# Performance work log

Measured on AMD Instinct MI355X. Metric: run time of the kernel, lower is better.

The kernel has to match this reference:

```python
import jax, jax.numpy as jnp
import numpy as np
from jax import lax

# PSTConv constants (match init_kwargs)
R = 0.5            # ball-query radius
K = 32             # neighbors per anchor
SPATIAL_STRIDE = 2
TK = 3             # temporal kernel size (odd)
TSTRIDE = 1        # temporal stride
PAD = (1, 1)       # temporal padding, 'zeros' mode
MID = 128
OUT = 256


def setup_inputs() -> dict:
    key = jax.random.key(0)
    k1, k2, k3, k4, k5 = jax.random.split(key, 5)
    B, L, N, C = 8, 6, 2048, 64
    xyzs = jax.random.uniform(k1, (B, L, N, 3), dtype=jnp.float32)
    features = jax.random.normal(k2, (B, L, C, N), dtype=jnp.float32)
    # kaiming_uniform with size=[mid, in+3, 1, 1]: bound = 1/sqrt(in_planes+3)
    b = 1.0 / np.sqrt(C + 3)
    w_d = jax.random.uniform(k3, (MID, 3), minval=-b, maxval=b, dtype=jnp.float32)
    w_f = jax.random.uniform(k4, (MID, C), minval=-b, maxval=b, dtype=jnp.float32)
    bt = 1.0 / np.sqrt(TK * MID)
    w_t = jax.random.uniform(k5, (OUT, TK * MID), minval=-bt, maxval=bt, dtype=jnp.float32)
    return {"xyzs": xyzs, "features": features, "w_d": w_d, "w_f": w_f, "w_t": w_t}


def _fps(xyz, m):
    # furthest point sampling on [N,3]; CUDA kernel starts from index 0
    N = xyz.shape[0]
    def step(carry, _):
        dists, far = carry
        d = jnp.sum((xyz - xyz[far]) ** 2, axis=-1)
        dists = jnp.minimum(dists, d)
        nxt = jnp.argmax(dists).astype(jnp.int32)
        return (dists, nxt), far
    init = (jnp.full((N,), 1e10, dtype=xyz.dtype), jnp.int32(0))
    _, idx = lax.scan(step, init, None, length=m)
    return idx  # [m] int32


def _ball_query(nbr_xyz, anchor_xyz):
    # nbr_xyz [B,N,3], anchor_xyz [B,M,3] -> [B,M,K] int32 indices into N
    # Semantics of pointnet2 ball_query: first K points (in index order) within
    # radius R; slots past the count are filled with the first found index
    # (0 if no point is in range).
    N = nbr_xyz.shape[1]
    d2 = jnp.sum((anchor_xyz[:, :, None, :] - nbr_xyz[:, None, :, :]) ** 2, axis=-1)  # [B,M,N]
    vals = jnp.where(d2 < R * R, jnp.arange(N, dtype=jnp.int32), jnp.int32(N))
    neg_top, _ = lax.top_k(-vals, K)          # K smallest indices, ascending
    idx = -neg_top                            # [B,M,K]
    first = idx[..., :1]
    fill = jnp.where(first < N, first, 0)
    return jnp.where(idx < N, idx, fill)


def _group(feat, idx):
    # feat [B,C,N], idx [B,M,K] -> [B,C,M,K]
    return jax.vmap(lambda f, i: f[:, i])(feat, idx)


def reference(xyzs, features, w_d, w_f, w_t):
    B, L, N, _ = xyzs.shape
    M = N // SPATIAL_STRIDE
    rad = TK // 2
    # zero temporal padding
    zx = jnp.zeros((B, 1, N, 3), xyzs.dtype)
    zf = jnp.zeros((B, 1, features.shape[2], N), features.dtype)
    xp = jnp.concatenate([zx] * PAD[0] + [xyzs] + [zx] * PAD[1], axis=1)
    fp = jnp.concatenate([zf] * PAD[0] + [features] + [zf] * PAD[1], axis=1)
    Lp = L + PAD[0] + PAD[1]

    new_xyzs, new_feats = [], []
    fps_b = jax.vmap(lambda x: _fps(x, M))
    for t in range(rad, Lp - rad, TSTRIDE):
        xyz_t = xp[:, t]                                   # [B,N,3]
        aidx = fps_b(xyz_t)                                # [B,M]
        anchor = jnp.take_along_axis(xyz_t, aidx[:, :, None], axis=1)  # [B,M,3]
        anchor_c = jnp.transpose(anchor, (0, 2, 1))[:, :, :, None]     # [B,3,M,1]
        sfs = []
        for i in range(t - rad, t + rad + 1):
            idx = _ball_query(xp[:, i], anchor)            # [B,M,K]
            g_xyz = _group(jnp.transpose(xp[:, i], (0, 2, 1)), idx)    # [B,3,M,K]
            disp = g_xyz - anchor_c
            d = jnp.einsum('oc,bcmk->bomk', w_d, disp)     # [B,MID,M,K]
            g_f = _group(fp[:, i], idx)                    # [B,C,M,K]
            f = jnp.einsum('oc,bcmk->bomk', w_f, g_f)
            sfs.append(jnp.max(f + d, axis=-1))            # [B,MID,M]
        sf = jax.nn.relu(jnp.concatenate(sfs, axis=1))     # [B,TK*MID,M]
        new_feats.append(jnp.einsum('oc,bcm->bom', w_t, sf))
        new_xyzs.append(anchor)
    return jnp.stack(new_xyzs, axis=1), jnp.stack(new_feats, axis=1)
```

## Files before the change

kernel.cpp:

```cpp
#include <hip/hip_runtime.h>

#define BATCH 8
#define LFRM  6
#define NP    2048
#define MP    1024
#define CIN   64
#define MIDC  128
#define OUTC  256
#define TKM   384
#define KNN   32
#define RAD2  0.25f

#define FPS_BLOCKS (BATCH * LFRM)
#define FT_BLOCKS  (BATCH * LFRM * (NP / 64))
#define WFS 132

typedef float f2 __attribute__((ext_vector_type(2)));
typedef float f32x4 __attribute__((ext_vector_type(4)));
typedef _Float16 f16x8 __attribute__((ext_vector_type(8)));
typedef _Float16 f16x4 __attribute__((ext_vector_type(4)));

union SharedU {
  struct {
    float4 pts[NP];
    unsigned long long wk[2][4];
  } fps;
  struct {
    float ftile[CIN][64];
    float wfT[CIN][WFS];
    float xt[64], yt[64], zt[64];
    float wdl[MIDC * 3];
  } ft;
};

__device__ __forceinline__ uint64_t kmax64(uint64_t a, uint64_t b) {
  return a > b ? a : b;
}
template <int CTRL>
__device__ __forceinline__ uint64_t key_dpp(uint64_t k) {
  int lo = __builtin_amdgcn_update_dpp((int)(uint32_t)k, (int)(uint32_t)k,
                                       CTRL, 0xF, 0xF, false);
  int hi = __builtin_amdgcn_update_dpp((int)(uint32_t)(k >> 32),
                                       (int)(uint32_t)(k >> 32),
                                       CTRL, 0xF, 0xF, false);
  return ((uint64_t)(uint32_t)hi << 32) | (uint32_t)lo;
}
__device__ __forceinline__ uint64_t key_swz16(uint64_t k) {
  int lo = __builtin_amdgcn_ds_swizzle((int)(uint32_t)k, 0x401F);
  int hi = __builtin_amdgcn_ds_swizzle((int)(uint32_t)(k >> 32), 0x401F);
  return ((uint64_t)(uint32_t)hi << 32) | (uint32_t)lo;
}
__device__ __forceinline__ uint64_t key_x32(uint64_t k) {
  int lo = __shfl_xor((int)(uint32_t)k, 32);
  int hi = __shfl_xor((int)(uint32_t)(k >> 32), 32);
  return ((uint64_t)(uint32_t)hi << 32) | (uint32_t)lo;
}

__device__ __forceinline__ void fps_path(const float* __restrict__ xyzs,
                                         float* __restrict__ out_xyz,
                                         SharedU* sh) {
#pragma clang fp contract(off)
  const int bt = blockIdx.x;
  const int tid = threadIdx.x;
  const int lane = tid & 63, wv = tid >> 6;
  const float* src = xyzs + (size_t)bt * NP * 3;

  for (int q = tid; q < NP; q += 256)
    sh->fps.pts[q] = make_float4(src[q * 3 + 0], src[q * 3 + 1], src[q * 3 + 2], 0.f);
  __syncthreads();

  f2 px[4], py[4], pz[4], dist[4];
#pragma unroll
  for (int u = 0; u < 4; ++u) {
    float4 a = sh->fps.pts[(wv * 8 + 2 * u) * 64 + lane];
    float4 b = sh->fps.pts[(wv * 8 + 2 * u + 1) * 64 + lane];
    px[u] = f2{a.x, b.x};
    py[u] = f2{a.y, b.y};
    pz[u] = f2{a.z, b.z};
    dist[u] = f2{1e10f, 1e10f};
  }

  float4 p0 = sh->fps.pts[0];
  float fx = p0.x, fy = p0.y, fz = p0.z;
  float* dst = out_xyz + (size_t)bt * MP * 3;

  for (int it = 0; it < MP; ++it) {
    if (tid == 0) {
      dst[it * 3 + 0] = fx;
      dst[it * 3 + 1] = fy;
      dst[it * 3 + 2] = fz;
    }
    const f2 fx2 = {fx, fx}, fy2 = {fy, fy}, fz2 = {fz, fz};
    float bv = -1.0f;
    int bsu = 0;
#pragma unroll
    for (int u = 0; u < 4; ++u) {
      f2 dx = px[u] - fx2;
      f2 dy = py[u] - fy2;
      f2 dz = pz[u] - fz2;
      f2 m = dx * dx;
      m = m + dy * dy;
      m = m + dz * dz;
      f2 nd = __builtin_elementwise_min(dist[u], m);
      dist[u] = nd;
      bool cx = nd.x > bv;
      bv = cx ? nd.x : bv;
      bsu = cx ? 2 * u : bsu;
      bool cy = nd.y > bv;
      bv = cy ? nd.y : bv;
      bsu = cy ? 2 * u + 1 : bsu;
    }
    const uint32_t p = (uint32_t)(((wv * 8 + bsu) << 6) | lane);
    uint64_t key = ((uint64_t)__float_as_uint(bv) << 32) | (uint32_t)(~p);
    key = kmax64(key, key_dpp<0x121>(key));
    key = kmax64(key, key_dpp<0x122>(key));
    key = kmax64(key, key_dpp<0x124>(key));
    key = kmax64(key, key_dpp<0x128>(key));
    key = kmax64(key, key_swz16(key));
    key = kmax64(key, key_x32(key));

    const int par = it & 1;
    if (lane == 0) sh->fps.wk[par][wv] = key;
    __syncthreads();
    uint64_t k0 = kmax64(sh->fps.wk[par][0], sh->fps.wk[par][1]);
    uint64_t k1 = kmax64(sh->fps.wk[par][2], sh->fps.wk[par][3]);
    uint64_t kg = kmax64(k0, k1);
    const uint32_t wp = ~(uint32_t)kg;
    float4 w = sh->fps.pts[wp];
    fx = w.x; fy = w.y; fz = w.z;
  }
}

__device__ __forceinline__ void ftrans_path(const float* __restrict__ features,
                                            const float* __restrict__ w_f,
                                            const float* __restrict__ w_d,
                                            const float* __restrict__ xyzs,
                                            float* __restrict__ G,
                                            SharedU* sh) {
  const int blk = blockIdx.x - FPS_BLOCKS;
  const int ntile = blk & 31;
  const int bl = blk >> 5;
  const int tid = threadIdx.x;

  const float* fsrc = features + (size_t)bl * CIN * NP + (size_t)ntile * 64;
  for (int idx = tid; idx < CIN * 64; idx += 256) {
    int c = idx >> 6, n = idx & 63;
    sh->ft.ftile[c][n] = fsrc[(size_t)c * NP + n];
  }
  for (int idx = tid; idx < CIN * MIDC; idx += 256) {
    int c = idx & 63, o = idx >> 6;
    sh->ft.wfT[c][o] = w_f[o * CIN + c];
  }
  if (tid < 64) {
    const float* xs = xyzs + ((size_t)bl * NP + (size_t)ntile * 64 + tid) * 3;
    sh->ft.xt[tid] = xs[0];
    sh->ft.yt[tid] = xs[1];
    sh->ft.zt[tid] = xs[2];
  }
  for (int idx = tid; idx < MIDC * 3; idx += 256) sh->ft.wdl[idx] = w_d[idx];
  __syncthreads();

  const int op = tid & 31;
  const int ng = tid >> 5;
  const int ob = op * 4;
  const int nb = ng * 8;

  float acc[4][8];
#pragma unroll
  for (int oo = 0; oo < 4; ++oo) {
    const float w0 = sh->ft.wdl[(ob + oo) * 3 + 0];
    const float w1 = sh->ft.wdl[(ob + oo) * 3 + 1];
    const float w2 = sh->ft.wdl[(ob + oo) * 3 + 2];
#pragma unroll
    for (int j = 0; j < 8; ++j)
      acc[oo][j] = w0 * sh->ft.xt[nb + j] + w1 * sh->ft.yt[nb + j] +
                   w2 * sh->ft.zt[nb + j];
  }

#pragma unroll 4
  for (int c = 0; c < CIN; ++c) {
    const float4 wq = *(const float4*)&sh->ft.wfT[c][ob];
    const float4 fA = *(const float4*)&sh->ft.ftile[c][nb];
    const float4 fB = *(const float4*)&sh->ft.ftile[c][nb + 4];
    const float wo[4] = {wq.x, wq.y, wq.z, wq.w};
    const float fv[8] = {fA.x, fA.y, fA.z, fA.w, fB.x, fB.y, fB.z, fB.w};
#pragma unroll
    for (int oo = 0; oo < 4; ++oo)
#pragma unroll
      for (int j = 0; j < 8; ++j)
        acc[oo][j] += wo[oo] * fv[j];
  }

  float* dstp = G + ((size_t)bl * NP + (size_t)ntile * 64) * MIDC;
#pragma unroll
  for (int j = 0; j < 8; ++j) {
    float4 v = make_float4(acc[0][j], acc[1][j], acc[2][j], acc[3][j]);
    *(float4*)&dstp[(size_t)(nb + j) * MIDC + ob] = v;
  }
}

__global__ __launch_bounds__(256, 1) void fps_ftrans_kernel(
    const float* __restrict__ xyzs, const float* __restrict__ features,
    const float* __restrict__ w_f, const float* __restrict__ w_d,
    float* __restrict__ out_xyz, float* __restrict__ G) {
  __shared__ SharedU sh;
  if (blockIdx.x < FPS_BLOCKS) {
    fps_path(xyzs, out_xyz, &sh);
    return;
  }
  ftrans_path(features, w_f, w_d, xyzs, G, &sh);
}

#define PSTR 392

__global__ __launch_bounds__(256) void pst_main(const float* __restrict__ xyzs,
                                                const float* __restrict__ w_d,
                                                const float* __restrict__ w_t,
                                                const float* __restrict__ G,
                                                const float* __restrict__ anchors,
                                                float* __restrict__ out_feat) {
  __shared__ union {
    float pxyz[NP * 3];
    _Float16 sf[32][PSTR];
  } u;
  __shared__ unsigned short nidx[32][KNN];
  __shared__ float anc[32][3];

  const int blk = blockIdx.x;
  const int mt = blk & 31;
  const int bt = blk >> 5;
  const int b = bt / LFRM;
  const int t = bt % LFRM + 1;
  const int tid = threadIdx.x;

  const float* asrc = anchors + ((size_t)bt * MP + (size_t)mt * 32) * 3;
  if (tid < 96) anc[tid / 3][tid % 3] = asrc[tid];
  __syncthreads();

  const int al = tid >> 3;
  const int j = tid & 7;
  const float ax = anc[al][0], ay = anc[al][1], az = anc[al][2];

  float wda[16];
#pragma unroll
  for (int c4 = 0; c4 < 4; ++c4)
#pragma unroll
    for (int r = 0; r < 4; ++r) {
      int o = c4 * 32 + j * 4 + r;
      wda[c4 * 4 + r] = w_d[o * 3 + 0] * ax + w_d[o * 3 + 1] * ay +
                        w_d[o * 3 + 2] * az;
    }

  const int lane = tid & 63, wv = tid >> 6;

  f16x4 hreg[3][4];

#pragma unroll
  for (int ii = 0; ii < 3; ++ii) {
    const int i = t - 1 + ii;

    if (i == 0 || i == LFRM + 1) {
#pragma unroll
      for (int c4 = 0; c4 < 4; ++c4) {
        f16x4 h;
#pragma unroll
        for (int r = 0; r < 4; ++r)
          h[r] = (_Float16)fmaxf(-wda[c4 * 4 + r], 0.f);
        hreg[ii][c4] = h;
      }
    } else {
      const int f2i = i - 1;
      const float* fxyz = xyzs + (size_t)(b * LFRM + f2i) * NP * 3;
      __syncthreads();
      for (int q = tid; q < NP * 3; q += 256) u.pxyz[q] = fxyz[q];
      __syncthreads();

      for (int aa = 0; aa < 8; ++aa) {
        const int a = wv * 8 + aa;
        const float qx = anc[a][0], qy = anc[a][1], qz = anc[a][2];
        int total = 0;
        int fillidx = 0;
        for (int ch = 0; ch < NP / 64; ++ch) {
          const int p = ch * 64 + lane;
          float d2;
          {
#pragma clang fp contract(off)
            float dx = qx - u.pxyz[p * 3 + 0];
            float dy = qy - u.pxyz[p * 3 + 1];
            float dz = qz - u.pxyz[p * 3 + 2];
            d2 = dx * dx + dy * dy + dz * dz;
          }
          const bool inb = d2 < RAD2;
          const unsigned long long mk = __ballot(inb);
          if (mk != 0ull && total == 0)
            fillidx = ch * 64 + (int)__builtin_ctzll(mk);
          const int before = (int)__builtin_popcountll(mk & ((1ull << lane) - 1ull));
          const int slot = total + before;
          if (inb && slot < KNN) nidx[a][slot] = (unsigned short)p;
          total += (int)__builtin_popcountll(mk);
          if (total >= KNN) break;
        }
        const int nf = total < KNN ? total : KNN;
        if (lane < KNN - nf) nidx[a][nf + lane] = (unsigned short)fillidx;
      }

      const float* gf = G + (size_t)(b * LFRM + f2i) * NP * MIDC;
      float mg[16];
#pragma unroll
      for (int uq = 0; uq < 16; ++uq) mg[uq] = -1e30f;
#pragma unroll 4
      for (int k = 0; k < KNN; ++k) {
        const int p = nidx[al][k];
        const float* rowp = gf + (size_t)p * MIDC + j * 4;
#pragma unroll
        for (int c4 = 0; c4 < 4; ++c4) {
          float4 v = *(const float4*)(rowp + c4 * 32);
          mg[c4 * 4 + 0] = fmaxf(mg[c4 * 4 + 0], v.x);
          mg[c4 * 4 + 1] = fmaxf(mg[c4 * 4 + 1], v.y);
          mg[c4 * 4 + 2] = fmaxf(mg[c4 * 4 + 2], v.z);
          mg[c4 * 4 + 3] = fmaxf(mg[c4 * 4 + 3], v.w);
        }
      }
#pragma unroll
      for (int c4 = 0; c4 < 4; ++c4) {
        f16x4 h;
#pragma unroll
        for (int r = 0; r < 4; ++r)
          h[r] = (_Float16)fmaxf(mg[c4 * 4 + r] - wda[c4 * 4 + r], 0.f);
        hreg[ii][c4] = h;
      }
    }
  }

  __syncthreads();
#pragma unroll
  for (int ii = 0; ii < 3; ++ii)
#pragma unroll
    for (int c4 = 0; c4 < 4; ++c4)
      *(f16x4*)&u.sf[al][ii * MIDC + c4 * 32 + j * 4] = hreg[ii][c4];
  __syncthreads();

  const int l16 = lane & 15, lq = lane >> 4;
  f32x4 accm[4][2];
#pragma unroll
  for (int q = 0; q < 4; ++q)
#pragma unroll
    for (int n2 = 0; n2 < 2; ++n2) accm[q][n2] = f32x4{0.f, 0.f, 0.f, 0.f};

  for (int kc = 0; kc < TKM / 32; ++kc) {
    f16x8 bfr[2];
#pragma unroll
    for (int n2 = 0; n2 < 2; ++n2)
      bfr[n2] = *(const f16x8*)&u.sf[n2 * 16 + l16][kc * 32 + lq * 8];
#pragma unroll
    for (int q = 0; q < 4; ++q) {
      const int row = (wv * 4 + q) * 16 + l16;
      const float4* ap = (const float4*)(w_t + (size_t)row * TKM + kc * 32 + lq * 8);
      float4 a0 = ap[0], a1 = ap[1];
      f16x8 afr;
      afr[0] = (_Float16)a0.x; afr[1] = (_Float16)a0.y;
      afr[2] = (_Float16)a0.z; afr[3] = (_Float16)a0.w;
      afr[4] = (_Float16)a1.x; afr[5] = (_Float16)a1.y;
      afr[6] = (_Float16)a1.z; afr[7] = (_Float16)a1.w;
      accm[q][0] = __builtin_amdgcn_mfma_f32_16x16x32_f16(afr, bfr[0], accm[q][0], 0, 0, 0);
      accm[q][1] = __builtin_amdgcn_mfma_f32_16x16x32_f16(afr, bfr[1], accm[q][1], 0, 0, 0);
    }
  }

  float* ob = out_feat + (size_t)bt * OUTC * MP + (size_t)mt * 32;
#pragma unroll
  for (int q = 0; q < 4; ++q) {
    const int orow = (wv * 4 + q) * 16 + lq * 4;
#pragma unroll
    for (int n2 = 0; n2 < 2; ++n2)
#pragma unroll
      for (int r = 0; r < 4; ++r)
        ob[(size_t)(orow + r) * MP + n2 * 16 + l16] = accm[q][n2][r];
  }
}

extern "C" void kernel_launch(void* const* d_in, const int* in_sizes, int n_in,
                              void* d_out, int out_size, void* d_ws, size_t ws_size,
                              hipStream_t stream) {
  const float* xyzs = (const float*)d_in[0];
  const float* features = (const float*)d_in[1];
  const float* w_d = (const float*)d_in[2];
  const float* w_f = (const float*)d_in[3];
  const float* w_t = (const float*)d_in[4];

  float* out = (float*)d_out;
  float* out_xyz = out;
  float* out_feat = out + (size_t)BATCH * LFRM * MP * 3;
  float* G = (float*)d_ws;

  hipLaunchKernelGGL(fps_ftrans_kernel, dim3(FPS_BLOCKS + FT_BLOCKS), dim3(256),
                     0, stream, xyzs, features, w_f, w_d, out_xyz, G);
  hipLaunchKernelGGL(pst_main, dim3(BATCH * LFRM * (MP / 32)), dim3(256), 0,
                     stream, xyzs, w_d, w_t, G, out_xyz, out_feat);
}
```

Baseline: 648.7 us.

## Store transformed features and temporal weights in fp16, reduce FPS with DPP row broadcasts

The per-point transformed feature buffer G is now written and gathered in fp16, which halves the traffic of the neighbor gather-max in the main kernel, and the max and subtract are done with packed half vectors. The temporal weights are converted to fp16 once by extra blocks in the first kernel, so the MFMA loop loads ready-made half fragments instead of converting fp32 each time. The FPS wave reduction replaces the swizzle and shuffle steps with DPP row-broadcast steps and reads the result from lane 63. The cost is lower precision in the gathered features and in the w_d-anchor offset, which could change results near ties.

```diff
diff --git a/kernel.cpp b/kernel.cpp
--- a/kernel.cpp
+++ b/kernel.cpp
@@ -12,6 +12,7 @@
 #define RAD2  0.25f
 
 #define FPS_BLOCKS (BATCH * LFRM)
+#define WT_BLOCKS  ((OUTC * TKM) / (256 * 4))
 #define FT_BLOCKS  (BATCH * LFRM * (NP / 64))
 #define WFS 132
 
@@ -45,15 +46,14 @@
                                        CTRL, 0xF, 0xF, false);
   return ((uint64_t)(uint32_t)hi << 32) | (uint32_t)lo;
 }
-__device__ __forceinline__ uint64_t key_swz16(uint64_t k) {
-  int lo = __builtin_amdgcn_ds_swizzle((int)(uint32_t)k, 0x401F);
-  int hi = __builtin_amdgcn_ds_swizzle((int)(uint32_t)(k >> 32), 0x401F);
-  return ((uint64_t)(uint32_t)hi << 32) | (uint32_t)lo;
-}
-__device__ __forceinline__ uint64_t key_x32(uint64_t k) {
-  int lo = __shfl_xor((int)(uint32_t)k, 32);
-  int hi = __shfl_xor((int)(uint32_t)(k >> 32), 32);
-  return ((uint64_t)(uint32_t)hi << 32) | (uint32_t)lo;
+
+__device__ __forceinline__ f16x4 h4max(f16x4 a, f16x4 b) {
+  f16x4 r;
+  r[0] = a[0] > b[0] ? a[0] : b[0];
+  r[1] = a[1] > b[1] ? a[1] : b[1];
+  r[2] = a[2] > b[2] ? a[2] : b[2];
+  r[3] = a[3] > b[3] ? a[3] : b[3];
+  return r;
 }
 
 __device__ __forceinline__ void fps_path(const float* __restrict__ xyzs,
@@ -116,11 +116,11 @@
     key = kmax64(key, key_dpp<0x122>(key));
     key = kmax64(key, key_dpp<0x124>(key));
     key = kmax64(key, key_dpp<0x128>(key));
-    key = kmax64(key, key_swz16(key));
-    key = kmax64(key, key_x32(key));
+    key = kmax64(key, key_dpp<0x142>(key));
+    key = kmax64(key, key_dpp<0x143>(key));
 
     const int par = it & 1;
-    if (lane == 0) sh->fps.wk[par][wv] = key;
+    if (lane == 63) sh->fps.wk[par][wv] = key;
     __syncthreads();
     uint64_t k0 = kmax64(sh->fps.wk[par][0], sh->fps.wk[par][1]);
     uint64_t k1 = kmax64(sh->fps.wk[par][2], sh->fps.wk[par][3]);
@@ -131,13 +131,24 @@
   }
 }
 
+__device__ __forceinline__ void wt_path(const float* __restrict__ w_t,
+                                        _Float16* __restrict__ wtH) {
+  const int blk = blockIdx.x - FPS_BLOCKS;
+  const int idx = (blk * 256 + (int)threadIdx.x) * 4;
+  const float4 v = *(const float4*)&w_t[idx];
+  f16x4 h;
+  h[0] = (_Float16)v.x; h[1] = (_Float16)v.y;
+  h[2] = (_Float16)v.z; h[3] = (_Float16)v.w;
+  *(f16x4*)&wtH[idx] = h;
+}
+
 __device__ __forceinline__ void ftrans_path(const float* __restrict__ features,
                                             const float* __restrict__ w_f,
                                             const float* __restrict__ w_d,
                                             const float* __restrict__ xyzs,
-                                            float* __restrict__ G,
+                                            _Float16* __restrict__ G,
                                             SharedU* sh) {
-  const int blk = blockIdx.x - FPS_BLOCKS;
+  const int blk = blockIdx.x - FPS_BLOCKS - WT_BLOCKS;
   const int ntile = blk & 31;
   const int bl = blk >> 5;
   const int tid = threadIdx.x;
@@ -191,23 +202,30 @@
         acc[oo][j] += wo[oo] * fv[j];
   }
 
-  float* dstp = G + ((size_t)bl * NP + (size_t)ntile * 64) * MIDC;
+  _Float16* dstp = G + ((size_t)bl * NP + (size_t)ntile * 64) * MIDC;
 #pragma unroll
   for (int j = 0; j < 8; ++j) {
-    float4 v = make_float4(acc[0][j], acc[1][j], acc[2][j], acc[3][j]);
-    *(float4*)&dstp[(size_t)(nb + j) * MIDC + ob] = v;
+    f16x4 v;
+    v[0] = (_Float16)acc[0][j]; v[1] = (_Float16)acc[1][j];
+    v[2] = (_Float16)acc[2][j]; v[3] = (_Float16)acc[3][j];
+    *(f16x4*)&dstp[(size_t)(nb + j) * MIDC + ob] = v;
   }
 }
 
 __global__ __launch_bounds__(256, 1) void fps_ftrans_kernel(
     const float* __restrict__ xyzs, const float* __restrict__ features,
     const float* __restrict__ w_f, const float* __restrict__ w_d,
-    float* __restrict__ out_xyz, float* __restrict__ G) {
+    const float* __restrict__ w_t, float* __restrict__ out_xyz,
+    _Float16* __restrict__ G, _Float16* __restrict__ wtH) {
   __shared__ SharedU sh;
   if (blockIdx.x < FPS_BLOCKS) {
     fps_path(xyzs, out_xyz, &sh);
     return;
   }
+  if (blockIdx.x < FPS_BLOCKS + WT_BLOCKS) {
+    wt_path(w_t, wtH);
+    return;
+  }
   ftrans_path(features, w_f, w_d, xyzs, G, &sh);
 }
 
@@ -215,8 +233,8 @@
 
 __global__ __launch_bounds__(256) void pst_main(const float* __restrict__ xyzs,
                                                 const float* __restrict__ w_d,
-                                                const float* __restrict__ w_t,
-                                                const float* __restrict__ G,
+                                                const _Float16* __restrict__ wtH,
+                                                const _Float16* __restrict__ G,
                                                 const float* __restrict__ anchors,
                                                 float* __restrict__ out_feat) {
   __shared__ union {
@@ -241,15 +259,16 @@
   const int j = tid & 7;
   const float ax = anc[al][0], ay = anc[al][1], az = anc[al][2];
 
-  float wda[16];
+  f16x4 wdah[4];
 #pragma unroll
   for (int c4 = 0; c4 < 4; ++c4)
 #pragma unroll
     for (int r = 0; r < 4; ++r) {
       int o = c4 * 32 + j * 4 + r;
-      wda[c4 * 4 + r] = w_d[o * 3 + 0] * ax + w_d[o * 3 + 1] * ay +
-                        w_d[o * 3 + 2] * az;
+      wdah[c4][r] = (_Float16)(w_d[o * 3 + 0] * ax + w_d[o * 3 + 1] * ay +
+                               w_d[o * 3 + 2] * az);
     }
+  const f16x4 hz = {(_Float16)0.f, (_Float16)0.f, (_Float16)0.f, (_Float16)0.f};
 
   const int lane = tid & 63, wv = tid >> 6;
 
@@ -261,13 +280,8 @@
 
     if (i == 0 || i == LFRM + 1) {
 #pragma unroll
-      for (int c4 = 0; c4 < 4; ++c4) {
-        f16x4 h;
-#pragma unroll
-        for (int r = 0; r < 4; ++r)
-          h[r] = (_Float16)fmaxf(-wda[c4 * 4 + r], 0.f);
-        hreg[ii][c4] = h;
-      }
+      for (int c4 = 0; c4 < 4; ++c4)
+        hreg[ii][c4] = h4max(hz - wdah[c4], hz);
     } else {
       const int f2i = i - 1;
       const float* fxyz = xyzs + (size_t)(b * LFRM + f2i) * NP * 3;
@@ -304,31 +318,23 @@
         if (lane < KNN - nf) nidx[a][nf + lane] = (unsigned short)fillidx;
       }
 
-      const float* gf = G + (size_t)(b * LFRM + f2i) * NP * MIDC;
-      float mg[16];
-#pragma unroll
-      for (int uq = 0; uq < 16; ++uq) mg[uq] = -1e30f;
+      const _Float16* gfr = G + (size_t)(b * LFRM + f2i) * NP * MIDC;
+      f16x4 mh0 = {(_Float16)-6e4f, (_Float16)-6e4f, (_Float16)-6e4f, (_Float16)-6e4f};
+      f16x4 mh1 = mh0, mh2 = mh0, mh3 = mh0;
 #pragma unroll 4
       for (int k = 0; k < KNN; ++k) {
         const int p = nidx[al][k];
-        const float* rowp = gf + (size_t)p * MIDC + j * 4;
-#pragma unroll
-        for (int c4 = 0; c4 < 4; ++c4) {
-          float4 v = *(const float4*)(rowp + c4 * 32);
-          mg[c4 * 4 + 0] = fmaxf(mg[c4 * 4 + 0], v.x);
-          mg[c4 * 4 + 1] = fmaxf(mg[c4 * 4 + 1], v.y);
-          mg[c4 * 4 + 2] = fmaxf(mg[c4 * 4 + 2], v.z);
-          mg[c4 * 4 + 3] = fmaxf(mg[c4 * 4 + 3], v.w);
-        }
+        const f16x4* row = (const f16x4*)(gfr + (size_t)p * MIDC);
+        f16x4 v0 = row[j], v1 = row[8 + j], v2 = row[16 + j], v3 = row[24 + j];
+        mh0 = h4max(mh0, v0);
+        mh1 = h4max(mh1, v1);
+        mh2 = h4max(mh2, v2);
+        mh3 = h4max(mh3, v3);
       }
-#pragma unroll
-      for (int c4 = 0; c4 < 4; ++c4) {
-        f16x4 h;
-#pragma unroll
-        for (int r = 0; r < 4; ++r)
-          h[r] = (_Float16)fmaxf(mg[c4 * 4 + r] - wda[c4 * 4 + r], 0.f);
-        hreg[ii][c4] = h;
-      }
+      hreg[ii][0] = h4max(mh0 - wdah[0], hz);
+      hreg[ii][1] = h4max(mh1 - wdah[1], hz);
+      hreg[ii][2] = h4max(mh2 - wdah[2], hz);
+      hreg[ii][3] = h4max(mh3 - wdah[3], hz);
     }
   }
 
@@ -355,13 +361,7 @@
 #pragma unroll
     for (int q = 0; q < 4; ++q) {
       const int row = (wv * 4 + q) * 16 + l16;
-      const float4* ap = (const float4*)(w_t + (size_t)row * TKM + kc * 32 + lq * 8);
-      float4 a0 = ap[0], a1 = ap[1];
-      f16x8 afr;
-      afr[0] = (_Float16)a0.x; afr[1] = (_Float16)a0.y;
-      afr[2] = (_Float16)a0.z; afr[3] = (_Float16)a0.w;
-      afr[4] = (_Float16)a1.x; afr[5] = (_Float16)a1.y;
-      afr[6] = (_Float16)a1.z; afr[7] = (_Float16)a1.w;
+      const f16x8 afr = *(const f16x8*)&wtH[(size_t)row * TKM + kc * 32 + lq * 8];
       accm[q][0] = __builtin_amdgcn_mfma_f32_16x16x32_f16(afr, bfr[0], accm[q][0], 0, 0, 0);
       accm[q][1] = __builtin_amdgcn_mfma_f32_16x16x32_f16(afr, bfr[1], accm[q][1], 0, 0, 0);
     }
@@ -391,10 +391,12 @@
   float* out = (float*)d_out;
   float* out_xyz = out;
   float* out_feat = out + (size_t)BATCH * LFRM * MP * 3;
-  float* G = (float*)d_ws;
-
-  hipLaunchKernelGGL(fps_ftrans_kernel, dim3(FPS_BLOCKS + FT_BLOCKS), dim3(256),
-                     0, stream, xyzs, features, w_f, w_d, out_xyz, G);
+  _Float16* G = (_Float16*)d_ws;
+  _Float16* wtH = G + (size_t)BATCH * LFRM * NP * MIDC;
+
+  hipLaunchKernelGGL(fps_ftrans_kernel,
+                     dim3(FPS_BLOCKS + WT_BLOCKS + FT_BLOCKS), dim3(256),
+                     0, stream, xyzs, features, w_f, w_d, w_t, out_xyz, G, wtH);
   hipLaunchKernelGGL(pst_main, dim3(BATCH * LFRM * (MP / 32)), dim3(256), 0,
-                     stream, xyzs, w_d, w_t, G, out_xyz, out_feat);
-}
+                     stream, xyzs, w_d, wtH, G, out_xyz, out_feat);
+}
```

After: 580.4 us. 10.5% less time.
